# Optimization experiments

Hardware: AMD Instinct MI355X
Metric: run time of the kernel (lower is better)

## Reference

```python
import jax, jax.numpy as jnp
import numpy as np

N = 200000   # active voxels
C = 128      # in_channels == out_channels -> identity downsample
K = 27       # 3x3x3 kernel offsets
EPS = 1e-5


def setup_inputs() -> dict:
    key = jax.random.key(0)
    ks = jax.random.split(key, 4)
    x = jax.random.normal(ks[0], (N, C), jnp.float32)
    nbr = jax.random.randint(ks[1], (N, K), 0, N, jnp.int32)
    W1 = jax.random.normal(ks[2], (K, C, C), jnp.float32) * 0.05
    W2 = jax.random.normal(ks[3], (K, C, C), jnp.float32) * 0.05
    g1 = jnp.ones((C,), jnp.float32); b1 = jnp.zeros((C,), jnp.float32)
    g2 = jnp.ones((C,), jnp.float32); b2 = jnp.zeros((C,), jnp.float32)
    return {"x": x, "nbr": nbr, "W1": W1, "g1": g1, "b1": b1,
            "W2": W2, "g2": g2, "b2": b2}


def _sparse_conv(x, nbr, W):
    # gather-matmul-scatter sparse conv: out[i] = sum_k W[k]^T x[nbr[i,k]]
    # scan over the K=27 kernel offsets to avoid materializing [N,K,C].
    def body(acc, kn):
        Wk, nk = kn                               # [C,C], [N]
        return acc + jnp.take(x, nk, axis=0) @ Wk, None
    acc0 = jnp.zeros((x.shape[0], W.shape[2]), x.dtype)
    out, _ = jax.lax.scan(body, acc0, (W, nbr.T))
    return out


def _bn(x, g, b):
    # training-mode batch norm over the point dimension
    m = jnp.mean(x, axis=0)
    v = jnp.var(x, axis=0)
    return (x - m) * jax.lax.rsqrt(v + EPS) * g + b


def reference(x, nbr, W1, g1, b1, W2, g2, b2):
    out = jax.nn.relu(_bn(_sparse_conv(x, nbr, W1), g1, b1))
    out = _bn(_sparse_conv(out, nbr, W2), g2, b2)
    # downsample is identity (in_channels == out_channels, stride == 1)
    return jax.nn.relu(out + x)
```

## Files before the change

kernel.cpp:

```cpp
#include <hip/hip_runtime.h>
#include <hip/hip_bf16.h>
#include <stdint.h>

#define C_DIM 128
#define K_DIM 27

typedef __attribute__((ext_vector_type(8))) short short8;
typedef __attribute__((ext_vector_type(4))) float f32x4;
typedef __attribute__((ext_vector_type(4))) unsigned short ushort4v;

#define VMCNT8() asm volatile("s_waitcnt vmcnt(8)" ::: "memory")
#define VMCNT4() asm volatile("s_waitcnt vmcnt(4)" ::: "memory")
#define VMCNT0() asm volatile("s_waitcnt vmcnt(0)" ::: "memory")
#define LGKM0() asm volatile("s_waitcnt lgkmcnt(0)" ::: "memory")
#define BAR() __builtin_amdgcn_s_barrier()

__device__ __forceinline__ unsigned short f2bf(float f) {
  unsigned int u = __builtin_bit_cast(unsigned int, f);
  u += 0x7fffu + ((u >> 16) & 1u);
  return (unsigned short)(u >> 16);
}
__device__ __forceinline__ float bf2f(unsigned short h) {
  unsigned int u = ((unsigned int)h) << 16;
  return __builtin_bit_cast(float, u);
}

__device__ __forceinline__ void async_copy16(const void* gsrc, void* ldst) {
  __builtin_amdgcn_global_load_lds(
      (const __attribute__((address_space(1))) unsigned int*)gsrc,
      (__attribute__((address_space(3))) unsigned int*)ldst, 16, 0, 0);
}

__global__ __launch_bounds__(256) void prep_kernel(
    const float* __restrict__ W1, const float* __restrict__ W2,
    unsigned short* __restrict__ Wt1, unsigned short* __restrict__ Wt2,
    float* __restrict__ stats, int stats_n) {
  int idx = blockIdx.x * 256 + threadIdx.x;
  const int total = K_DIM * C_DIM * C_DIM;
  if (idx < total) {
    int cq = idx & 31;
    int co = (idx >> 5) & 127;
    int q  = (idx >> 12) & 3;
    int k  = idx >> 14;
    int ci = q * 32 + cq;
    int src = (k * C_DIM + ci) * C_DIM + co;
    Wt1[idx] = f2bf(W1[src]);
    Wt2[idx] = f2bf(W2[src]);
  }
  if (idx < stats_n) stats[idx] = 0.f;
}

__global__ __launch_bounds__(256) void cvt_x_kernel(
    const float* __restrict__ x, unsigned short* __restrict__ xb, int total4) {
  int i = blockIdx.x * 256 + threadIdx.x;
  if (i >= total4) return;
  f32x4 v = ((const f32x4*)x)[i];
  ushort4v u;
#pragma unroll
  for (int j = 0; j < 4; ++j) u[j] = f2bf(v[j]);
  ((ushort4v*)xb)[i] = u;
}

template<int OUT_IS_F32>
__global__ __launch_bounds__(256, 2) void conv_kernel(
    const unsigned short* __restrict__ xb, const int* __restrict__ nbr,
    const unsigned short* __restrict__ Wt, void* __restrict__ out_v,
    float* __restrict__ stats, int N) {
  extern __shared__ __align__(16) char smem[];
  unsigned short* Abuf = (unsigned short*)smem;
  unsigned short* Wbuf = (unsigned short*)(smem + 32768);
  int* idx_lds = (int*)(smem + 65536);
  float* s_sum = (float*)(smem + 65536 + 13824);
  float* s_ssum = s_sum + C_DIM;

  const int tid = threadIdx.x;
  const int wave = tid >> 6, lane = tid & 63;
  const int lr = lane & 15, lg = lane >> 4;
  const int rg = wave >> 1, cg = wave & 1;
  const int row0 = blockIdx.x * 128;

  if (tid < C_DIM) { s_sum[tid] = 0.f; s_ssum[tid] = 0.f; }

  for (int i = tid; i < 128 * K_DIM; i += 256) {
    int r = i / K_DIM;
    int k = i - r * K_DIM;
    int rr = row0 + r; if (rr >= N) rr = N - 1;
    idx_lds[i] = nbr[(size_t)rr * K_DIM + k];
  }
  __syncthreads();

  const int gr = wave * 32 + (lane >> 2);
  const int gcol = (lane & 3) * 8;

  auto stage_a = [&](int gA, int gB, int q, int buf) {
    unsigned short* dst = Abuf + buf * 4096 + wave * 1024;
    async_copy16(xb + (size_t)gA * C_DIM + q * 32 + gcol, dst);
    async_copy16(xb + (size_t)gB * C_DIM + q * 32 + gcol, dst + 512);
  };
  auto stage_w = [&](int p, int buf) {
    const unsigned short* src = Wt + (size_t)p * 4096 + wave * 1024 + lane * 8;
    unsigned short* dst = Wbuf + buf * 4096 + wave * 1024;
    async_copy16(src, dst);
    async_copy16(src + 512, dst + 512);
  };

  f32x4 acc[4][4] = {};

  auto compute = [&](int buf) {
    const unsigned short* ab = Abuf + buf * 4096 + (rg * 64 + lr) * 32 + lg * 8;
    const unsigned short* wb = Wbuf + buf * 4096 + (cg * 64 + lr) * 32 + lg * 8;
    short8 a[4], b[4];
#pragma unroll
    for (int rt = 0; rt < 4; ++rt) a[rt] = *(const short8*)(ab + rt * 512);
#pragma unroll
    for (int ct = 0; ct < 4; ++ct) b[ct] = *(const short8*)(wb + ct * 512);
    __builtin_amdgcn_s_setprio(1);
#pragma unroll
    for (int rt = 0; rt < 4; ++rt)
#pragma unroll
      for (int ct = 0; ct < 4; ++ct)
        acc[rt][ct] = __builtin_amdgcn_mfma_f32_16x16x32_bf16(a[rt], b[ct], acc[rt][ct], 0, 0, 0);
    __builtin_amdgcn_s_setprio(0);
  };

  int gA = idx_lds[gr * K_DIM];
  int gB = idx_lds[(gr + 16) * K_DIM];
  LGKM0();
  stage_a(gA, gB, 0, 0); stage_w(0, 0);
  stage_a(gA, gB, 1, 1); stage_w(1, 1);
  stage_a(gA, gB, 2, 2); stage_w(2, 2);
  VMCNT8();
  BAR();

  for (int base = 0; base < 104; base += 4) {
    const int k1 = (base >> 2) + 1;
    int hA, hB;
    stage_a(gA, gB, 3, 3); stage_w(base + 3, 3);
    hA = idx_lds[gr * K_DIM + k1];
    hB = idx_lds[(gr + 16) * K_DIM + k1];
    compute(0);
    LGKM0(); VMCNT8(); BAR();
    stage_a(hA, hB, 0, 0); stage_w(base + 4, 0);
    compute(1);
    LGKM0(); VMCNT8(); BAR();
    stage_a(hA, hB, 1, 1); stage_w(base + 5, 1);
    compute(2);
    LGKM0(); VMCNT8(); BAR();
    stage_a(hA, hB, 2, 2); stage_w(base + 6, 2);
    compute(3);
    LGKM0(); VMCNT8(); BAR();
    gA = hA; gB = hB;
  }

  stage_a(gA, gB, 3, 3); stage_w(107, 3);
  compute(0);
  LGKM0(); VMCNT8(); BAR();
  compute(1);
  LGKM0(); VMCNT4(); BAR();
  compute(2);
  LGKM0(); VMCNT0(); BAR();
  compute(3);

  __syncthreads();
  float* ctile = (float*)smem;
  float ps[4] = {0.f, 0.f, 0.f, 0.f}, pss[4] = {0.f, 0.f, 0.f, 0.f};
#pragma unroll
  for (int rt = 0; rt < 4; ++rt) {
#pragma unroll
    for (int j = 0; j < 4; ++j) {
      int lrow = rg * 64 + rt * 16 + lg * 4 + j;
      bool ok = (row0 + lrow) < N;
#pragma unroll
      for (int ct = 0; ct < 4; ++ct) {
        float v = acc[rt][ct][j];
        ctile[lrow * C_DIM + cg * 64 + ct * 16 + lr] = v;
        if (ok) { ps[ct] += v; pss[ct] += v * v; }
      }
    }
  }
#pragma unroll
  for (int ct = 0; ct < 4; ++ct) {
    ps[ct]  += __shfl_xor(ps[ct], 16, 64);
    ps[ct]  += __shfl_xor(ps[ct], 32, 64);
    pss[ct] += __shfl_xor(pss[ct], 16, 64);
    pss[ct] += __shfl_xor(pss[ct], 32, 64);
    if (lg == 0) {
      int col = cg * 64 + ct * 16 + lr;
      atomicAdd(&s_sum[col], ps[ct]);
      atomicAdd(&s_ssum[col], pss[ct]);
    }
  }
  __syncthreads();
  if (tid < C_DIM) {
    atomicAdd(&stats[tid], s_sum[tid]);
    atomicAdd(&stats[C_DIM + tid], s_ssum[tid]);
  }
  for (int i = tid; i < 4096; i += 256) {
    int row = i >> 5;
    int c4 = i & 31;
    int grow = row0 + row;
    if (grow >= N) continue;
    f32x4 v = ((const f32x4*)ctile)[i];
    if (OUT_IS_F32) {
      ((f32x4*)out_v)[(size_t)grow * 32 + c4] = v;
    } else {
      ushort4v u;
#pragma unroll
      for (int j = 0; j < 4; ++j) u[j] = f2bf(v[j]);
      ((ushort4v*)out_v)[(size_t)grow * 32 + c4] = u;
    }
  }
}

__global__ void finalize_kernel(const float* __restrict__ stats,
                                const float* __restrict__ g,
                                const float* __restrict__ b,
                                float* __restrict__ sshift, float invN) {
  int c = threadIdx.x;
  float mean = stats[c] * invN;
  float var = stats[128 + c] * invN - mean * mean;
  float sc = g[c] * rsqrtf(var + 1e-5f);
  sshift[c] = sc;
  sshift[128 + c] = b[c] - mean * sc;
}

__global__ __launch_bounds__(256) void apply_kernel(
    unsigned short* __restrict__ y, const float* __restrict__ ss, int total8) {
  int i = blockIdx.x * 256 + threadIdx.x;
  if (i >= total8) return;
  int cb = (i * 8) & 127;
  short8 u = ((short8*)y)[i];
#pragma unroll
  for (int j = 0; j < 8; ++j) {
    float f = bf2f((unsigned short)u[j]) * ss[cb + j] + ss[128 + cb + j];
    u[j] = (short)f2bf(fmaxf(f, 0.f));
  }
  ((short8*)y)[i] = u;
}

__global__ __launch_bounds__(256) void final_kernel(
    float* __restrict__ y2, const float* __restrict__ x,
    const float* __restrict__ ss, int total4) {
  int i = blockIdx.x * 256 + threadIdx.x;
  if (i >= total4) return;
  int cb = (i * 4) & 127;
  f32x4 v = ((const f32x4*)y2)[i];
  f32x4 xv = ((const f32x4*)x)[i];
#pragma unroll
  for (int j = 0; j < 4; ++j)
    v[j] = fmaxf(v[j] * ss[cb + j] + ss[128 + cb + j] + xv[j], 0.f);
  ((f32x4*)y2)[i] = v;
}

extern "C" void kernel_launch(void* const* d_in, const int* in_sizes, int n_in,
                              void* d_out, int out_size, void* d_ws, size_t ws_size,
                              hipStream_t stream) {
  const float* x  = (const float*)d_in[0];
  const int* nbr  = (const int*)d_in[1];
  const float* W1 = (const float*)d_in[2];
  const float* g1 = (const float*)d_in[3];
  const float* b1 = (const float*)d_in[4];
  const float* W2 = (const float*)d_in[5];
  const float* g2 = (const float*)d_in[6];
  const float* b2 = (const float*)d_in[7];
  float* out = (float*)d_out;

  const int N = in_sizes[0] / C_DIM;
  const int totalW = K_DIM * C_DIM * C_DIM;
  const int SMEM_BYTES = 65536 + 13824 + 1024;

  char* ws = (char*)d_ws;
  size_t off = 0;
  auto alloc = [&](size_t bytes) {
    void* p = ws + off;
    off = (off + bytes + 255) & ~(size_t)255;
    return p;
  };
  unsigned short* Wt1 = (unsigned short*)alloc((size_t)totalW * 2);
  unsigned short* Wt2 = (unsigned short*)alloc((size_t)totalW * 2);
  float* stats = (float*)alloc(512 * 4);
  float* ss1   = (float*)alloc(256 * 4);
  float* ss2   = (float*)alloc(256 * 4);
  unsigned short* y1 = (unsigned short*)alloc((size_t)N * C_DIM * 2);
  unsigned short* xb_ws = (unsigned short*)alloc((size_t)N * C_DIM * 2);
  unsigned short* xb = (off <= ws_size) ? xb_ws : (unsigned short*)d_out;

  (void)hipFuncSetAttribute((const void*)conv_kernel<0>,
      hipFuncAttributeMaxDynamicSharedMemorySize, SMEM_BYTES);
  (void)hipFuncSetAttribute((const void*)conv_kernel<1>,
      hipFuncAttributeMaxDynamicSharedMemorySize, SMEM_BYTES);

  const int nblk = (N + 127) / 128;
  const float invN = 1.0f / (float)N;

  prep_kernel<<<(totalW + 255) / 256, 256, 0, stream>>>(W1, W2, Wt1, Wt2, stats, 512);

  {
    int t4 = N * C_DIM / 4;
    cvt_x_kernel<<<(t4 + 255) / 256, 256, 0, stream>>>(x, xb, t4);
  }

  conv_kernel<0><<<nblk, 256, SMEM_BYTES, stream>>>(xb, nbr, Wt1, y1, stats, N);
  finalize_kernel<<<1, 128, 0, stream>>>(stats, g1, b1, ss1, invN);

  {
    int t8 = N * C_DIM / 8;
    apply_kernel<<<(t8 + 255) / 256, 256, 0, stream>>>(y1, ss1, t8);
  }

  conv_kernel<1><<<nblk, 256, SMEM_BYTES, stream>>>(y1, nbr, Wt2, out, stats + 256, N);
  finalize_kernel<<<1, 128, 0, stream>>>(stats + 256, g2, b2, ss2, invN);

  {
    int t4 = N * C_DIM / 4;
    final_kernel<<<(t4 + 255) / 256, 256, 0, stream>>>(out, x, ss2, t4);
  }
}
```

Before: 582.9 us.

## Load conv weights directly into registers, swizzle A tile, write outputs from accumulators

Weight tiles are no longer staged through LDS. Each wave now loads its B fragments straight from global memory into double-buffered registers one stage ahead. This halves the LDS footprint, so launch bounds rise to 3 blocks per CU. An XOR swizzle on the gathered A tile aims to cut LDS bank conflicts, and the output epilogue writes accumulators directly to global memory instead of round-tripping through an LDS tile. The risks are extra register pressure from 8 short8 weight registers and less coalesced scalar output stores.

```diff
diff --git a/kernel.cpp b/kernel.cpp
--- a/kernel.cpp
+++ b/kernel.cpp
@@ -10,6 +10,7 @@
 typedef __attribute__((ext_vector_type(4))) unsigned short ushort4v;
 
 #define VMCNT8() asm volatile("s_waitcnt vmcnt(8)" ::: "memory")
+#define VMCNT6() asm volatile("s_waitcnt vmcnt(6)" ::: "memory")
 #define VMCNT4() asm volatile("s_waitcnt vmcnt(4)" ::: "memory")
 #define VMCNT0() asm volatile("s_waitcnt vmcnt(0)" ::: "memory")
 #define LGKM0() asm volatile("s_waitcnt lgkmcnt(0)" ::: "memory")
@@ -62,15 +63,14 @@
 }
 
 template<int OUT_IS_F32>
-__global__ __launch_bounds__(256, 2) void conv_kernel(
+__global__ __launch_bounds__(256, 3) void conv_kernel(
     const unsigned short* __restrict__ xb, const int* __restrict__ nbr,
     const unsigned short* __restrict__ Wt, void* __restrict__ out_v,
     float* __restrict__ stats, int N) {
   extern __shared__ __align__(16) char smem[];
   unsigned short* Abuf = (unsigned short*)smem;
-  unsigned short* Wbuf = (unsigned short*)(smem + 32768);
-  int* idx_lds = (int*)(smem + 65536);
-  float* s_sum = (float*)(smem + 65536 + 13824);
+  int* idx_lds = (int*)(smem + 32768);
+  float* s_sum = (float*)(smem + 32768 + 13824);
   float* s_ssum = s_sum + C_DIM;
 
   const int tid = threadIdx.x;
@@ -89,92 +89,116 @@
   }
   __syncthreads();
 
-  const int gr = wave * 32 + (lane >> 2);
-  const int gcol = (lane & 3) * 8;
-
-  auto stage_a = [&](int gA, int gB, int q, int buf) {
+  const int srow = lane >> 2;
+  const int ssw = ((lane & 3) ^ (srow & 3)) << 3;
+  const int gr0 = wave * 32 + srow;
+  const int gr1 = gr0 + 16;
+
+  auto stage = [&](int a0i, int a1i, int q, int buf) {
     unsigned short* dst = Abuf + buf * 4096 + wave * 1024;
-    async_copy16(xb + (size_t)gA * C_DIM + q * 32 + gcol, dst);
-    async_copy16(xb + (size_t)gB * C_DIM + q * 32 + gcol, dst + 512);
+    async_copy16(xb + (size_t)a0i * C_DIM + q * 32 + ssw, dst);
+    async_copy16(xb + (size_t)a1i * C_DIM + q * 32 + ssw, dst + 512);
   };
-  auto stage_w = [&](int p, int buf) {
-    const unsigned short* src = Wt + (size_t)p * 4096 + wave * 1024 + lane * 8;
-    unsigned short* dst = Wbuf + buf * 4096 + wave * 1024;
-    async_copy16(src, dst);
-    async_copy16(src + 512, dst + 512);
+
+  const unsigned short* wbase = Wt + (size_t)(cg * 64 + lr) * 32 + lg * 8;
+  short8 wE[4], wO[4];
+  auto wload = [&](short8 (&w)[4], int p) {
+    const unsigned short* wp = wbase + (size_t)p * 4096;
+#pragma unroll
+    for (int ct = 0; ct < 4; ++ct)
+      w[ct] = *(const short8*)(wp + ct * 512);
   };
 
   f32x4 acc[4][4] = {};
-
-  auto compute = [&](int buf) {
-    const unsigned short* ab = Abuf + buf * 4096 + (rg * 64 + lr) * 32 + lg * 8;
-    const unsigned short* wb = Wbuf + buf * 4096 + (cg * 64 + lr) * 32 + lg * 8;
-    short8 a[4], b[4];
-#pragma unroll
-    for (int rt = 0; rt < 4; ++rt) a[rt] = *(const short8*)(ab + rt * 512);
-#pragma unroll
-    for (int ct = 0; ct < 4; ++ct) b[ct] = *(const short8*)(wb + ct * 512);
+  const unsigned short* abase =
+      Abuf + (rg * 64 + lr) * 32 + ((lg ^ (lr & 3)) << 3);
+
+  auto compute = [&](const unsigned short* ab, const short8 (&w)[4]) {
+    short8 a[4];
+#pragma unroll
+    for (int rt = 0; rt < 4; ++rt)
+      a[rt] = *(const short8*)(ab + rt * 512);
     __builtin_amdgcn_s_setprio(1);
 #pragma unroll
     for (int rt = 0; rt < 4; ++rt)
 #pragma unroll
       for (int ct = 0; ct < 4; ++ct)
-        acc[rt][ct] = __builtin_amdgcn_mfma_f32_16x16x32_bf16(a[rt], b[ct], acc[rt][ct], 0, 0, 0);
+        acc[rt][ct] = __builtin_amdgcn_mfma_f32_16x16x32_bf16(a[rt], w[ct], acc[rt][ct], 0, 0, 0);
     __builtin_amdgcn_s_setprio(0);
   };
 
-  int gA = idx_lds[gr * K_DIM];
-  int gB = idx_lds[(gr + 16) * K_DIM];
-  LGKM0();
-  stage_a(gA, gB, 0, 0); stage_w(0, 0);
-  stage_a(gA, gB, 1, 1); stage_w(1, 1);
-  stage_a(gA, gB, 2, 2); stage_w(2, 2);
+  int gA = idx_lds[gr0 * K_DIM];
+  int gB = idx_lds[gr1 * K_DIM];
+  stage(gA, gB, 0, 0);
+  wload(wE, 0);
+  stage(gA, gB, 1, 1);
+  stage(gA, gB, 2, 2);
   VMCNT8();
   BAR();
 
   for (int base = 0; base < 104; base += 4) {
     const int k1 = (base >> 2) + 1;
     int hA, hB;
-    stage_a(gA, gB, 3, 3); stage_w(base + 3, 3);
-    hA = idx_lds[gr * K_DIM + k1];
-    hB = idx_lds[(gr + 16) * K_DIM + k1];
-    compute(0);
-    LGKM0(); VMCNT8(); BAR();
-    stage_a(hA, hB, 0, 0); stage_w(base + 4, 0);
-    compute(1);
-    LGKM0(); VMCNT8(); BAR();
-    stage_a(hA, hB, 1, 1); stage_w(base + 5, 1);
-    compute(2);
-    LGKM0(); VMCNT8(); BAR();
-    stage_a(hA, hB, 2, 2); stage_w(base + 6, 2);
-    compute(3);
-    LGKM0(); VMCNT8(); BAR();
+    wload(wO, base + 1);
+    stage(gA, gB, 3, 3);
+    hA = idx_lds[gr0 * K_DIM + k1];
+    hB = idx_lds[gr1 * K_DIM + k1];
+    VMCNT8();
+    compute(abase, wE);
+    LGKM0(); BAR();
+    wload(wE, base + 2);
+    stage(hA, hB, 0, 0);
+    VMCNT8();
+    compute(abase + 4096, wO);
+    LGKM0(); BAR();
+    wload(wO, base + 3);
+    stage(hA, hB, 1, 1);
+    VMCNT8();
+    compute(abase + 8192, wE);
+    LGKM0(); BAR();
+    wload(wE, base + 4);
+    stage(hA, hB, 2, 2);
+    VMCNT8();
+    compute(abase + 12288, wO);
+    LGKM0(); BAR();
     gA = hA; gB = hB;
   }
 
-  stage_a(gA, gB, 3, 3); stage_w(107, 3);
-  compute(0);
-  LGKM0(); VMCNT8(); BAR();
-  compute(1);
-  LGKM0(); VMCNT4(); BAR();
-  compute(2);
-  LGKM0(); VMCNT0(); BAR();
-  compute(3);
-
-  __syncthreads();
-  float* ctile = (float*)smem;
+  wload(wO, 105);
+  stage(gA, gB, 3, 3);
+  VMCNT8();
+  compute(abase, wE);
+  LGKM0(); BAR();
+  wload(wE, 106);
+  VMCNT6();
+  compute(abase + 4096, wO);
+  LGKM0(); BAR();
+  wload(wO, 107);
+  VMCNT4();
+  compute(abase + 8192, wE);
+  LGKM0(); BAR();
+  VMCNT0();
+  compute(abase + 12288, wO);
+
   float ps[4] = {0.f, 0.f, 0.f, 0.f}, pss[4] = {0.f, 0.f, 0.f, 0.f};
 #pragma unroll
   for (int rt = 0; rt < 4; ++rt) {
 #pragma unroll
     for (int j = 0; j < 4; ++j) {
-      int lrow = rg * 64 + rt * 16 + lg * 4 + j;
-      bool ok = (row0 + lrow) < N;
+      int grow = row0 + rg * 64 + rt * 16 + lg * 4 + j;
+      bool ok = grow < N;
 #pragma unroll
       for (int ct = 0; ct < 4; ++ct) {
         float v = acc[rt][ct][j];
-        ctile[lrow * C_DIM + cg * 64 + ct * 16 + lr] = v;
-        if (ok) { ps[ct] += v; pss[ct] += v * v; }
+        if (ok) {
+          int col = cg * 64 + ct * 16 + lr;
+          if (OUT_IS_F32)
+            ((float*)out_v)[(size_t)grow * C_DIM + col] = v;
+          else
+            ((unsigned short*)out_v)[(size_t)grow * C_DIM + col] = f2bf(v);
+          ps[ct] += v;
+          pss[ct] += v * v;
+        }
       }
     }
   }
@@ -194,21 +218,6 @@
   if (tid < C_DIM) {
     atomicAdd(&stats[tid], s_sum[tid]);
     atomicAdd(&stats[C_DIM + tid], s_ssum[tid]);
-  }
-  for (int i = tid; i < 4096; i += 256) {
-    int row = i >> 5;
-    int c4 = i & 31;
-    int grow = row0 + row;
-    if (grow >= N) continue;
-    f32x4 v = ((const f32x4*)ctile)[i];
-    if (OUT_IS_F32) {
-      ((f32x4*)out_v)[(size_t)grow * 32 + c4] = v;
-    } else {
-      ushort4v u;
-#pragma unroll
-      for (int j = 0; j < 4; ++j) u[j] = f2bf(v[j]);
-      ((ushort4v*)out_v)[(size_t)grow * 32 + c4] = u;
-    }
   }
 }
 
@@ -267,7 +276,7 @@
 
   const int N = in_sizes[0] / C_DIM;
   const int totalW = K_DIM * C_DIM * C_DIM;
-  const int SMEM_BYTES = 65536 + 13824 + 1024;
+  const int SMEM_BYTES = 32768 + 13824 + 1024;
 
   char* ws = (char*)d_ws;
   size_t off = 0;
@@ -285,11 +294,6 @@
   unsigned short* xb_ws = (unsigned short*)alloc((size_t)N * C_DIM * 2);
   unsigned short* xb = (off <= ws_size) ? xb_ws : (unsigned short*)d_out;
 
-  (void)hipFuncSetAttribute((const void*)conv_kernel<0>,
-      hipFuncAttributeMaxDynamicSharedMemorySize, SMEM_BYTES);
-  (void)hipFuncSetAttribute((const void*)conv_kernel<1>,
-      hipFuncAttributeMaxDynamicSharedMemorySize, SMEM_BYTES);
-
   const int nblk = (N + 127) / 128;
   const float invN = 1.0f / (float)N;
 
```

Result: slower. 656.4 us (+12.6%).

## Split activations into channel-quarter planes, swizzle LDS, reorder K loop, drop epilogue staging

Applied to the files above, without the earlier changes.

Activations are stored as four channel-quarter planes [q][N][32], and the conv loop now runs over quarters outermost and kernel offsets innermost, so each gather phase reads one plane. The gather is meant to stay within a smaller working set for better cache reuse. LDS tiles use an XOR swizzle, matched by reordering the weights in prep, to cut bank conflicts. The conv epilogue writes results straight from registers with nontemporal stores instead of going through an LDS tile, and the second conv writes bf16 into a workspace buffer. The x conversion is folded into the prep kernel, at the cost of scattered 2-byte stores in the epilogue and extra index math in apply and final.

```diff
diff --git a/kernel.cpp b/kernel.cpp
--- a/kernel.cpp
+++ b/kernel.cpp
@@ -4,6 +4,7 @@
 
 #define C_DIM 128
 #define K_DIM 27
+#define NPH (K_DIM * 4)
 
 typedef __attribute__((ext_vector_type(8))) short short8;
 typedef __attribute__((ext_vector_type(4))) float f32x4;
@@ -34,36 +35,45 @@
 __global__ __launch_bounds__(256) void prep_kernel(
     const float* __restrict__ W1, const float* __restrict__ W2,
     unsigned short* __restrict__ Wt1, unsigned short* __restrict__ Wt2,
-    float* __restrict__ stats, int stats_n) {
-  int idx = blockIdx.x * 256 + threadIdx.x;
-  const int total = K_DIM * C_DIM * C_DIM;
-  if (idx < total) {
-    int cq = idx & 31;
-    int co = (idx >> 5) & 127;
-    int q  = (idx >> 12) & 3;
-    int k  = idx >> 14;
-    int ci = q * 32 + cq;
-    int src = (k * C_DIM + ci) * C_DIM + co;
-    Wt1[idx] = f2bf(W1[src]);
-    Wt2[idx] = f2bf(W2[src]);
-  }
-  if (idx < stats_n) stats[idx] = 0.f;
-}
-
-__global__ __launch_bounds__(256) void cvt_x_kernel(
-    const float* __restrict__ x, unsigned short* __restrict__ xb, int total4) {
-  int i = blockIdx.x * 256 + threadIdx.x;
-  if (i >= total4) return;
-  f32x4 v = ((const f32x4*)x)[i];
-  ushort4v u;
-#pragma unroll
-  for (int j = 0; j < 4; ++j) u[j] = f2bf(v[j]);
-  ((ushort4v*)xb)[i] = u;
-}
-
-template<int OUT_IS_F32>
+    const float* __restrict__ x, unsigned short* __restrict__ xq,
+    float* __restrict__ stats, int N, int nWblk) {
+  if ((int)blockIdx.x < nWblk) {
+    int idx = blockIdx.x * 256 + threadIdx.x;
+    const int total = K_DIM * C_DIM * C_DIM;
+    if (idx < total) {
+      int e = idx & 7;
+      int gpos = (idx >> 3) & 3;
+      int co = (idx >> 5) & 127;
+      int p = idx >> 12;
+      int q = p / K_DIM, k = p - q * K_DIM;
+      int ci = q * 32 + ((gpos ^ ((co >> 1) & 3)) << 3) + e;
+      int src = (k * C_DIM + ci) * C_DIM + co;
+      Wt1[idx] = f2bf(W1[src]);
+      Wt2[idx] = f2bf(W2[src]);
+    }
+    if (idx < 512) stats[idx] = 0.f;
+  } else {
+    int t = ((int)blockIdx.x - nWblk) * 256 + threadIdx.x;
+    int total8 = N * 16;
+    if (t >= total8) return;
+    int flat = t * 8;
+    int row = flat >> 7;
+    int e = flat & 127;
+    int q = e >> 5, off = e & 31;
+    f32x4 v0 = ((const f32x4*)x)[t * 2];
+    f32x4 v1 = ((const f32x4*)x)[t * 2 + 1];
+    ushort4v u0, u1;
+#pragma unroll
+    for (int j = 0; j < 4; ++j) { u0[j] = f2bf(v0[j]); u1[j] = f2bf(v1[j]); }
+    unsigned short* dst = xq + ((size_t)q * N + row) * 32 + off;
+    *(ushort4v*)dst = u0;
+    *(ushort4v*)(dst + 4) = u1;
+  }
+}
+
+template<int OUT_LINEAR>
 __global__ __launch_bounds__(256, 2) void conv_kernel(
-    const unsigned short* __restrict__ xb, const int* __restrict__ nbr,
+    const unsigned short* __restrict__ xq, const int* __restrict__ nbr,
     const unsigned short* __restrict__ Wt, void* __restrict__ out_v,
     float* __restrict__ stats, int N) {
   extern __shared__ __align__(16) char smem[];
@@ -89,92 +99,96 @@
   }
   __syncthreads();
 
-  const int gr = wave * 32 + (lane >> 2);
-  const int gcol = (lane & 3) * 8;
-
-  auto stage_a = [&](int gA, int gB, int q, int buf) {
-    unsigned short* dst = Abuf + buf * 4096 + wave * 1024;
-    async_copy16(xb + (size_t)gA * C_DIM + q * 32 + gcol, dst);
-    async_copy16(xb + (size_t)gB * C_DIM + q * 32 + gcol, dst + 512);
+  const int srow = lane >> 2;
+  const int ssw = ((lane & 3) ^ ((srow >> 1) & 3)) << 3;
+  const int gr0 = wave * 32 + srow;
+  const int gr1 = gr0 + 16;
+
+  auto stage_a = [&](int sq, int sk, int sOff) {
+    int gi0 = idx_lds[gr0 * K_DIM + sk];
+    int gi1 = idx_lds[gr1 * K_DIM + sk];
+    const unsigned short* srcq = xq + (size_t)sq * N * 32 + ssw;
+    unsigned short* dst = Abuf + sOff + wave * 1024;
+    async_copy16(srcq + (size_t)gi0 * 32, dst);
+    async_copy16(srcq + (size_t)gi1 * 32, dst + 512);
   };
-  auto stage_w = [&](int p, int buf) {
+  auto stage_w = [&](int p, int sOff) {
     const unsigned short* src = Wt + (size_t)p * 4096 + wave * 1024 + lane * 8;
-    unsigned short* dst = Wbuf + buf * 4096 + wave * 1024;
+    unsigned short* dst = Wbuf + sOff + wave * 1024;
     async_copy16(src, dst);
     async_copy16(src + 512, dst + 512);
   };
 
   f32x4 acc[4][4] = {};
-
-  auto compute = [&](int buf) {
-    const unsigned short* ab = Abuf + buf * 4096 + (rg * 64 + lr) * 32 + lg * 8;
-    const unsigned short* wb = Wbuf + buf * 4096 + (cg * 64 + lr) * 32 + lg * 8;
-    short8 a[4], b[4];
-#pragma unroll
-    for (int rt = 0; rt < 4; ++rt) a[rt] = *(const short8*)(ab + rt * 512);
-#pragma unroll
-    for (int ct = 0; ct < 4; ++ct) b[ct] = *(const short8*)(wb + ct * 512);
+  const int swzr = (lg ^ ((lr >> 1) & 3)) << 3;
+  const int aro = (rg * 64 + lr) * 32 + swzr;
+  const int wro = (cg * 64 + lr) * 32 + swzr;
+
+  auto compute = [&](int cOff) {
+    short8 a_[4], b_[4];
+#pragma unroll
+    for (int rt = 0; rt < 4; ++rt)
+      a_[rt] = *(const short8*)(Abuf + cOff + aro + rt * 512);
+#pragma unroll
+    for (int ct = 0; ct < 4; ++ct)
+      b_[ct] = *(const short8*)(Wbuf + cOff + wro + ct * 512);
     __builtin_amdgcn_s_setprio(1);
 #pragma unroll
     for (int rt = 0; rt < 4; ++rt)
 #pragma unroll
       for (int ct = 0; ct < 4; ++ct)
-        acc[rt][ct] = __builtin_amdgcn_mfma_f32_16x16x32_bf16(a[rt], b[ct], acc[rt][ct], 0, 0, 0);
+        acc[rt][ct] = __builtin_amdgcn_mfma_f32_16x16x32_bf16(
+            a_[rt], b_[ct], acc[rt][ct], 0, 0, 0);
     __builtin_amdgcn_s_setprio(0);
   };
 
-  int gA = idx_lds[gr * K_DIM];
-  int gB = idx_lds[(gr + 16) * K_DIM];
-  LGKM0();
-  stage_a(gA, gB, 0, 0); stage_w(0, 0);
-  stage_a(gA, gB, 1, 1); stage_w(1, 1);
-  stage_a(gA, gB, 2, 2); stage_w(2, 2);
+  stage_a(0, 0, 0);     stage_w(0, 0);
+  stage_a(0, 1, 4096);  stage_w(1, 4096);
+  stage_a(0, 2, 8192);  stage_w(2, 8192);
   VMCNT8();
   BAR();
 
-  for (int base = 0; base < 104; base += 4) {
-    const int k1 = (base >> 2) + 1;
-    int hA, hB;
-    stage_a(gA, gB, 3, 3); stage_w(base + 3, 3);
-    hA = idx_lds[gr * K_DIM + k1];
-    hB = idx_lds[(gr + 16) * K_DIM + k1];
-    compute(0);
-    LGKM0(); VMCNT8(); BAR();
-    stage_a(hA, hB, 0, 0); stage_w(base + 4, 0);
-    compute(1);
-    LGKM0(); VMCNT8(); BAR();
-    stage_a(hA, hB, 1, 1); stage_w(base + 5, 1);
-    compute(2);
-    LGKM0(); VMCNT8(); BAR();
-    stage_a(hA, hB, 2, 2); stage_w(base + 6, 2);
-    compute(3);
-    LGKM0(); VMCNT8(); BAR();
-    gA = hA; gB = hB;
-  }
-
-  stage_a(gA, gB, 3, 3); stage_w(107, 3);
-  compute(0);
-  LGKM0(); VMCNT8(); BAR();
-  compute(1);
-  LGKM0(); VMCNT4(); BAR();
-  compute(2);
-  LGKM0(); VMCNT0(); BAR();
-  compute(3);
-
-  __syncthreads();
-  float* ctile = (float*)smem;
+  int sq = 0, sk = 3;
+  int cOff = 0, sOff = 12288;
+  for (int p = 0; p < NPH - 3; ++p) {
+    stage_a(sq, sk, sOff);
+    stage_w(sq * K_DIM + sk, sOff);
+    if (++sk == K_DIM) { sk = 0; ++sq; }
+    compute(cOff);
+    VMCNT8(); LGKM0(); BAR();
+    cOff = (cOff + 4096) & 16383;
+    sOff = (sOff + 4096) & 16383;
+  }
+  compute(cOff);
+  VMCNT4(); LGKM0(); BAR();
+  cOff = (cOff + 4096) & 16383;
+  compute(cOff);
+  VMCNT0(); LGKM0(); BAR();
+  cOff = (cOff + 4096) & 16383;
+  compute(cOff);
+
   float ps[4] = {0.f, 0.f, 0.f, 0.f}, pss[4] = {0.f, 0.f, 0.f, 0.f};
 #pragma unroll
   for (int rt = 0; rt < 4; ++rt) {
 #pragma unroll
     for (int j = 0; j < 4; ++j) {
-      int lrow = rg * 64 + rt * 16 + lg * 4 + j;
-      bool ok = (row0 + lrow) < N;
+      int grow = row0 + rg * 64 + rt * 16 + lg * 4 + j;
+      bool ok = grow < N;
 #pragma unroll
       for (int ct = 0; ct < 4; ++ct) {
         float v = acc[rt][ct][j];
-        ctile[lrow * C_DIM + cg * 64 + ct * 16 + lr] = v;
-        if (ok) { ps[ct] += v; pss[ct] += v * v; }
+        if (ok) {
+          int col = cg * 64 + ct * 16 + lr;
+          if (OUT_LINEAR) {
+            __builtin_nontemporal_store(
+                v, &((float*)out_v)[(size_t)grow * C_DIM + col]);
+          } else {
+            size_t a = ((size_t)(col >> 5) * N + grow) * 32 + (col & 31);
+            __builtin_nontemporal_store(f2bf(v), &((unsigned short*)out_v)[a]);
+          }
+          ps[ct] += v;
+          pss[ct] += v * v;
+        }
       }
     }
   }
@@ -195,21 +209,6 @@
     atomicAdd(&stats[tid], s_sum[tid]);
     atomicAdd(&stats[C_DIM + tid], s_ssum[tid]);
   }
-  for (int i = tid; i < 4096; i += 256) {
-    int row = i >> 5;
-    int c4 = i & 31;
-    int grow = row0 + row;
-    if (grow >= N) continue;
-    f32x4 v = ((const f32x4*)ctile)[i];
-    if (OUT_IS_F32) {
-      ((f32x4*)out_v)[(size_t)grow * 32 + c4] = v;
-    } else {
-      ushort4v u;
-#pragma unroll
-      for (int j = 0; j < 4; ++j) u[j] = f2bf(v[j]);
-      ((ushort4v*)out_v)[(size_t)grow * 32 + c4] = u;
-    }
-  }
 }
 
 __global__ void finalize_kernel(const float* __restrict__ stats,
@@ -225,10 +224,12 @@
 }
 
 __global__ __launch_bounds__(256) void apply_kernel(
-    unsigned short* __restrict__ y, const float* __restrict__ ss, int total8) {
+    unsigned short* __restrict__ y, const float* __restrict__ ss,
+    int N, int total8) {
   int i = blockIdx.x * 256 + threadIdx.x;
   if (i >= total8) return;
-  int cb = (i * 8) & 127;
+  int q = (i >> 2) / N;
+  int cb = q * 32 + ((i & 3) << 3);
   short8 u = ((short8*)y)[i];
 #pragma unroll
   for (int j = 0; j < 8; ++j) {
@@ -238,18 +239,33 @@
   ((short8*)y)[i] = u;
 }
 
+template<int IN_IS_QSPLIT>
 __global__ __launch_bounds__(256) void final_kernel(
-    float* __restrict__ y2, const float* __restrict__ x,
-    const float* __restrict__ ss, int total4) {
+    const void* __restrict__ y2_v, const float* __restrict__ x,
+    const float* __restrict__ ss, float* __restrict__ out, int N, int total4) {
   int i = blockIdx.x * 256 + threadIdx.x;
   if (i >= total4) return;
-  int cb = (i * 4) & 127;
-  f32x4 v = ((const f32x4*)y2)[i];
+  int flat = i * 4;
+  int cb = flat & 127;
+  f32x4 v;
+  if (IN_IS_QSPLIT) {
+    int row = flat >> 7;
+    int q = cb >> 5, off = cb & 31;
+    ushort4v u = *(const ushort4v*)(
+        (const unsigned short*)y2_v + ((size_t)q * N + row) * 32 + off);
+#pragma unroll
+    for (int j = 0; j < 4; ++j) v[j] = bf2f(u[j]);
+  } else {
+    v = ((const f32x4*)y2_v)[i];
+  }
   f32x4 xv = ((const f32x4*)x)[i];
 #pragma unroll
   for (int j = 0; j < 4; ++j)
     v[j] = fmaxf(v[j] * ss[cb + j] + ss[128 + cb + j] + xv[j], 0.f);
-  ((f32x4*)y2)[i] = v;
+  __builtin_nontemporal_store(v[0], &out[flat + 0]);
+  __builtin_nontemporal_store(v[1], &out[flat + 1]);
+  __builtin_nontemporal_store(v[2], &out[flat + 2]);
+  __builtin_nontemporal_store(v[3], &out[flat + 3]);
 }
 
 extern "C" void kernel_launch(void* const* d_in, const int* in_sizes, int n_in,
@@ -267,7 +283,7 @@
 
   const int N = in_sizes[0] / C_DIM;
   const int totalW = K_DIM * C_DIM * C_DIM;
-  const int SMEM_BYTES = 65536 + 13824 + 1024;
+  const int SMEM_BYTES = 32768 + 32768 + 13824 + 1024;
 
   char* ws = (char*)d_ws;
   size_t off = 0;
@@ -282,8 +298,11 @@
   float* ss1   = (float*)alloc(256 * 4);
   float* ss2   = (float*)alloc(256 * 4);
   unsigned short* y1 = (unsigned short*)alloc((size_t)N * C_DIM * 2);
-  unsigned short* xb_ws = (unsigned short*)alloc((size_t)N * C_DIM * 2);
-  unsigned short* xb = (off <= ws_size) ? xb_ws : (unsigned short*)d_out;
+  unsigned short* y2b = (unsigned short*)alloc((size_t)N * C_DIM * 2);
+  const bool use_y2b = (off <= ws_size);
+  unsigned short* xq_ws = (unsigned short*)alloc((size_t)N * C_DIM * 2);
+  const bool use_xq = (off <= ws_size);
+  unsigned short* xq = use_xq ? xq_ws : (unsigned short*)d_out;
 
   (void)hipFuncSetAttribute((const void*)conv_kernel<0>,
       hipFuncAttributeMaxDynamicSharedMemorySize, SMEM_BYTES);
@@ -292,27 +311,29 @@
 
   const int nblk = (N + 127) / 128;
   const float invN = 1.0f / (float)N;
-
-  prep_kernel<<<(totalW + 255) / 256, 256, 0, stream>>>(W1, W2, Wt1, Wt2, stats, 512);
+  const int nWblk = (totalW + 255) / 256;
+  const int nXblk = (N * 16 + 255) / 256;
+
+  prep_kernel<<<nWblk + nXblk, 256, 0, stream>>>(
+      W1, W2, Wt1, Wt2, x, xq, stats, N, nWblk);
+
+  conv_kernel<0><<<nblk, 256, SMEM_BYTES, stream>>>(xq, nbr, Wt1, y1, stats, N);
+  finalize_kernel<<<1, 128, 0, stream>>>(stats, g1, b1, ss1, invN);
+
+  apply_kernel<<<(N * 16 + 255) / 256, 256, 0, stream>>>(y1, ss1, N, N * 16);
+
+  if (use_y2b) {
+    conv_kernel<0><<<nblk, 256, SMEM_BYTES, stream>>>(y1, nbr, Wt2, y2b, stats + 256, N);
+  } else {
+    conv_kernel<1><<<nblk, 256, SMEM_BYTES, stream>>>(y1, nbr, Wt2, out, stats + 256, N);
+  }
+  finalize_kernel<<<1, 128, 0, stream>>>(stats + 256, g2, b2, ss2, invN);
 
   {
     int t4 = N * C_DIM / 4;
-    cvt_x_kernel<<<(t4 + 255) / 256, 256, 0, stream>>>(x, xb, t4);
-  }
-
-  conv_kernel<0><<<nblk, 256, SMEM_BYTES, stream>>>(xb, nbr, Wt1, y1, stats, N);
-  finalize_kernel<<<1, 128, 0, stream>>>(stats, g1, b1, ss1, invN);
-
-  {
-    int t8 = N * C_DIM / 8;
-    apply_kernel<<<(t8 + 255) / 256, 256, 0, stream>>>(y1, ss1, t8);
-  }
-
-  conv_kernel<1><<<nblk, 256, SMEM_BYTES, stream>>>(y1, nbr, Wt2, out, stats + 256, N);
-  finalize_kernel<<<1, 128, 0, stream>>>(stats + 256, g2, b2, ss2, invN);
-
-  {
-    int t4 = N * C_DIM / 4;
-    final_kernel<<<(t4 + 255) / 256, 256, 0, stream>>>(out, x, ss2, t4);
-  }
-}
+    if (use_y2b)
+      final_kernel<1><<<(t4 + 255) / 256, 256, 0, stream>>>(y2b, x, ss2, out, N, t4);
+    else
+      final_kernel<0><<<(t4 + 255) / 256, 256, 0, stream>>>(out, x, ss2, out, N, t4);
+  }
+}
```

Result: slower. 781.3 us (+34.0%).
